# Optimization experiments

Hardware: AMD Instinct MI355X
Metric: run time of the kernel (lower is better)

The kernel has to match this reference:

```python
import jax, jax.numpy as jnp
import numpy as np

HIDDEN = 800
BETA = 0.95
SLOPE = 25.0

@jax.custom_vjp
def surrogate_spike(mem, thr):
    # hard threshold forward, sigmoid-derivative surrogate backward
    return (mem > thr).astype(mem.dtype)

def _spk_fwd(mem, thr):
    return surrogate_spike(mem, thr), (mem, thr)

def _spk_bwd(res, g):
    mem, thr = res
    s = jax.nn.sigmoid(SLOPE * (mem - thr))
    return (g * SLOPE * s * (1.0 - s), jnp.zeros_like(thr))

surrogate_spike.defvjp(_spk_fwd, _spk_bwd)


def setup_inputs() -> dict:
    key = jax.random.key(0)
    ks = jax.random.split(key, 6)
    T, B = 50, 512
    x = jax.random.normal(ks[0], (T, B, 784), dtype=jnp.float32)
    # Kaiming-ish init scaled by 1/sqrt(fan_in)
    W1 = jax.random.normal(ks[1], (HIDDEN, 784), dtype=jnp.float32) / np.sqrt(784.0)
    W2 = jax.random.normal(ks[2], (HIDDEN, HIDDEN), dtype=jnp.float32) / np.sqrt(float(HIDDEN))
    W3 = jax.random.normal(ks[3], (10, HIDDEN), dtype=jnp.float32) / np.sqrt(float(HIDDEN))
    b1 = jnp.zeros((HIDDEN,), jnp.float32)
    b2 = jnp.zeros((HIDDEN,), jnp.float32)
    b3 = jnp.zeros((10,), jnp.float32)
    budget1 = jax.random.uniform(ks[4], (HIDDEN,), dtype=jnp.float32)
    budget2 = jax.random.uniform(ks[5], (HIDDEN,), dtype=jnp.float32)
    return {"x": x, "W1": W1, "b1": b1, "W2": W2, "b2": b2,
            "W3": W3, "b3": b3, "budget1": budget1, "budget2": budget2}


def reference(x, W1, b1, W2, b2, W3, b3, budget1, budget2):
    # thresholds: 1 / clamp(budget / max_budget, 0.01, 1.0); max_budget = 1.0 here
    thr1 = 1.0 / jnp.clip(budget1, 0.01, 1.0)
    thr2 = 1.0 / jnp.clip(budget2, 0.01, 1.0)
    thr3 = jnp.asarray(1.0, x.dtype)
    B = x.shape[1]

    def step(carry, xt):
        m1, m2, m3 = carry
        m1 = BETA * m1 + xt @ W1.T + b1            # [B, HIDDEN]
        s1 = surrogate_spike(m1, thr1)
        m1 = m1 * (1.0 - s1)                        # multiplicative reset
        m2 = BETA * m2 + s1 @ W2.T + b2
        s2 = surrogate_spike(m2, thr2)
        m2 = m2 * (1.0 - s2)
        m3 = BETA * m3 + s2 @ W3.T + b3            # [B, 10]
        s3 = surrogate_spike(m3, thr3)
        m3 = m3 * (1.0 - s3)
        return (m1, m2, m3), (s1, s2, s3)

    init = (jnp.zeros((B, HIDDEN), x.dtype),
            jnp.zeros((B, HIDDEN), x.dtype),
            jnp.zeros((B, 10), x.dtype))
    _, (s1r, s2r, s3r) = jax.lax.scan(step, init, x)
    return (s3r.sum(0), s1r, s2r, s3r)
```

## Files before the change

### kernel.cpp

```cpp
#include <hip/hip_runtime.h>

#define BATCH   512
#define TSTEPS  50
#define NIN     784
#define NHID    800
#define NOUT    10
#define KC      384

#define BM 128
#define BN 64
#define BK 8

__global__ __launch_bounds__(256, 4)
void gemm_nt_f32(const float* __restrict__ A, const float* __restrict__ B,
                 float* __restrict__ C, int M, int N, int K)
{
    __shared__ float As[BK][BM + 4];
    __shared__ float Bs[BK][BN + 4];

    const int tid = threadIdx.x;
    const int tx = tid & 15;
    const int ty = tid >> 4;
    const int m0 = blockIdx.x * BM;
    const int n0 = blockIdx.y * BN;

    const int arow = tid >> 1;
    const int akq  = (tid & 1) * 4;
    const int brow = tid >> 2;
    const int bkq  = (tid & 3) * 2;

    const float* Aptr = A + (size_t)(m0 + arow) * K + akq;
    const float* Bptr = B + (size_t)(n0 + brow) * K + bkq;
    const bool bval = (n0 + brow) < N;

    float part[8][4];
    float acc[8][4];
    #pragma unroll
    for (int i = 0; i < 8; ++i)
        #pragma unroll
        for (int j = 0; j < 4; ++j) part[i][j] = 0.0f;

    float4 av = *(const float4*)(Aptr);
    float2 bv = bval ? *(const float2*)(Bptr) : make_float2(0.f, 0.f);

    for (int k0 = 0; k0 < K; k0 += BK) {
        __syncthreads();
        As[akq+0][arow] = av.x; As[akq+1][arow] = av.y;
        As[akq+2][arow] = av.z; As[akq+3][arow] = av.w;
        Bs[bkq+0][brow] = bv.x; Bs[bkq+1][brow] = bv.y;
        __syncthreads();

        if (k0 + BK < K) {
            av = *(const float4*)(Aptr + k0 + BK);
            bv = bval ? *(const float2*)(Bptr + k0 + BK) : make_float2(0.f, 0.f);
        }

        if (k0 == 384 || k0 == 768) {
            #pragma unroll
            for (int i = 0; i < 8; ++i)
                #pragma unroll
                for (int j = 0; j < 4; ++j) {
                    acc[i][j] = (k0 == 384) ? part[i][j]
                                            : __fadd_rn(acc[i][j], part[i][j]);
                    part[i][j] = 0.0f;
                }
        }

        #pragma unroll
        for (int kk = 0; kk < BK; ++kk) {
            float a[8], b[4];
            *(float4*)&a[0] = *(const float4*)&As[kk][8*ty];
            *(float4*)&a[4] = *(const float4*)&As[kk][8*ty + 4];
            *(float4*)&b[0] = *(const float4*)&Bs[kk][4*tx];
            #pragma unroll
            for (int i = 0; i < 8; ++i)
                #pragma unroll
                for (int j = 0; j < 4; ++j)
                    part[i][j] = __fmaf_rn(a[i], b[j], part[i][j]);
        }
    }

    #pragma unroll
    for (int i = 0; i < 8; ++i)
        #pragma unroll
        for (int j = 0; j < 4; ++j)
            acc[i][j] = (K <= KC) ? part[i][j] : __fadd_rn(acc[i][j], part[i][j]);

    const int cb = n0 + 4*tx;
    #pragma unroll
    for (int i = 0; i < 8; ++i) {
        const int m = m0 + 8*ty + i;
        float* crow = C + (size_t)m * N + cb;
        if (cb + 3 < N) {
            *(float4*)crow = make_float4(acc[i][0], acc[i][1], acc[i][2], acc[i][3]);
        } else {
            #pragma unroll
            for (int j = 0; j < 4; ++j)
                if (cb + j < N) crow[j] = acc[i][j];
        }
    }
}

__global__ __launch_bounds__(256)
void transpose800(const float* __restrict__ W2, float* __restrict__ W2T)
{
    __shared__ float t[32][33];
    const int tx  = threadIdx.x & 31;
    const int ty8 = threadIdx.x >> 5;
    const int bx = blockIdx.x * 32, by = blockIdx.y * 32;

    #pragma unroll
    for (int r = 0; r < 4; ++r) {
        int a = ty8 + r * 8;
        t[a][tx] = W2[(size_t)(by + a) * 800 + bx + tx];
    }
    __syncthreads();
    #pragma unroll
    for (int r = 0; r < 4; ++r) {
        int a = ty8 + r * 8;
        W2T[(size_t)(bx + a) * 800 + by + tx] = t[tx][a];
    }
}

__global__ __launch_bounds__(256)
void lif_scan_hid(const float* __restrict__ Z,
                  const float* __restrict__ bias,
                  const float* __restrict__ budget,
                  float* __restrict__ mcarry,
                  float* __restrict__ Sout,
                  unsigned long long* __restrict__ bm,
                  int CT, int t0)
{
    const int b = blockIdx.x;
    const int tid = threadIdx.x;
    const int lane = tid & 63;
    const int wave = tid >> 6;

    float m[4], thr[4], bj[4];
    bool val[4];
    #pragma unroll
    for (int c = 0; c < 4; ++c) {
        const int j = c * 256 + tid;
        val[c] = (j < NHID);
        const int jj = val[c] ? j : 0;
        float bu = budget[jj];
        bu = fminf(fmaxf(bu, 0.01f), 1.0f);
        thr[c] = __fdiv_rn(1.0f, bu);
        bj[c]  = bias[jj];
        m[c]   = mcarry[b * NHID + jj];
    }

    for (int ct = 0; ct < CT; ++ct) {
        const size_t zbase = (size_t)ct * (BATCH * NHID) + (size_t)b * NHID;
        const size_t sbase = (size_t)(t0 + ct) * (BATCH * NHID) + (size_t)b * NHID;
        #pragma unroll
        for (int c = 0; c < 4; ++c) {
            const int j = c * 256 + tid;
            bool sp = false;
            if (val[c]) {
                float z = Z[zbase + j];
                float mm = __fadd_rn(__fadd_rn(__fmul_rn(0.95f, m[c]), z), bj[c]);
                sp = (mm > thr[c]);
                m[c] = sp ? 0.0f : mm;
                Sout[sbase + j] = sp ? 1.0f : 0.0f;
            }
            unsigned long long bits = __ballot(sp);
            if (bm && lane == 0) {
                const int W = c * 4 + wave;
                if (W < 13)
                    bm[((size_t)ct * BATCH + b) * 13 + W] = bits;
            }
        }
    }
    #pragma unroll
    for (int c = 0; c < 4; ++c)
        if (val[c]) mcarry[b * NHID + c * 256 + tid] = m[c];
}

__global__ __launch_bounds__(256)
void spmm_spikes(const unsigned long long* __restrict__ bm,
                 const float* __restrict__ W2T,
                 float* __restrict__ Z,
                 int rows)
{
    __shared__ unsigned long long wbuf[13];
    __shared__ unsigned short list[NHID];
    __shared__ int offs[14];

    const int tid = threadIdx.x;
    const int lane = tid & 63;
    const int wave = tid >> 6;
    const int row = blockIdx.x;

    if (tid < 13) wbuf[tid] = bm[(size_t)row * 13 + tid];
    __syncthreads();
    if (tid == 0) {
        int o = 0;
        for (int w = 0; w < 13; ++w) { offs[w] = o; o += __popcll(wbuf[w]); }
        offs[13] = o;
    }
    __syncthreads();
    for (int W = wave; W < 13; W += 4) {
        const unsigned long long bits = wbuf[W];
        const int pre = __popcll(bits & ((1ull << lane) - 1ull));
        if ((bits >> lane) & 1ull)
            list[offs[W] + pre] = (unsigned short)(W * 64 + lane);
    }
    __syncthreads();
    const int nnz = offs[13];

    if (tid < 200) {
        const int n = 4 * tid;
        float p0 = 0.f, p1 = 0.f, p2 = 0.f, p3 = 0.f;
        float a0 = 0.f, a1 = 0.f, a2 = 0.f, a3 = 0.f;
        int p = 0, nextb = KC;
        for (int i = 0; i < nnz; ++i) {
            const int k = list[i];
            while (k >= nextb) {
                if (p == 0) { a0 = p0; a1 = p1; a2 = p2; a3 = p3; }
                else {
                    a0 = __fadd_rn(a0, p0); a1 = __fadd_rn(a1, p1);
                    a2 = __fadd_rn(a2, p2); a3 = __fadd_rn(a3, p3);
                }
                p0 = p1 = p2 = p3 = 0.f; ++p;
                nextb = (nextb == KC) ? 2 * KC : 100000;
            }
            const float4 w = *(const float4*)(W2T + (size_t)k * NHID + n);
            p0 = __fadd_rn(p0, w.x); p1 = __fadd_rn(p1, w.y);
            p2 = __fadd_rn(p2, w.z); p3 = __fadd_rn(p3, w.w);
        }
        while (p < 3) {
            if (p == 0) { a0 = p0; a1 = p1; a2 = p2; a3 = p3; }
            else {
                a0 = __fadd_rn(a0, p0); a1 = __fadd_rn(a1, p1);
                a2 = __fadd_rn(a2, p2); a3 = __fadd_rn(a3, p3);
            }
            p0 = p1 = p2 = p3 = 0.f; ++p;
        }
        *(float4*)(Z + (size_t)row * NHID + n) = make_float4(a0, a1, a2, a3);
    }
}

__global__ __launch_bounds__(256)
void gemm3_f32(const float* __restrict__ S2, const float* __restrict__ W3,
               float* __restrict__ Z3, int rows)
{
    int gid = blockIdx.x * 256 + threadIdx.x;
    if (gid >= rows * NOUT) return;
    const int m = gid / NOUT;
    const int n = gid % NOUT;
    const float* a = S2 + (size_t)m * NHID;
    const float* w = W3 + (size_t)n * NHID;

    float acc = 0.0f;
    for (int p0 = 0; p0 < NHID; p0 += KC) {
        const int pend = (p0 + KC < NHID) ? (p0 + KC) : NHID;
        float part = 0.0f;
        for (int k = p0; k < pend; ++k)
            part = __fmaf_rn(a[k], w[k], part);
        acc = (p0 == 0) ? part : __fadd_rn(acc, part);
    }
    Z3[gid] = acc;
}

__global__ __launch_bounds__(256)
void lif_scan_small(const float* __restrict__ Z, const float* __restrict__ bias,
                    float* __restrict__ mcarry, float* __restrict__ Sout,
                    int CT, int t0)
{
    const int idx = blockIdx.x * blockDim.x + threadIdx.x;
    const int total = BATCH * NOUT;
    if (idx >= total) return;
    const int j = idx % NOUT;
    const float thr = 1.0f;
    const float bj = bias[j];

    float m = mcarry[idx];
    for (int ct = 0; ct < CT; ++ct) {
        float z = Z[(size_t)ct * total + idx];
        m = __fadd_rn(__fadd_rn(__fmul_rn(0.95f, m), z), bj);
        float s;
        if (m > thr) { s = 1.0f; m = 0.0f; }
        else         { s = 0.0f; }
        Sout[(size_t)(t0 + ct) * total + idx] = s;
    }
    mcarry[idx] = m;
}

__global__ __launch_bounds__(256)
void sum_t(const float* __restrict__ S3, float* __restrict__ out0)
{
    const int idx = blockIdx.x * blockDim.x + threadIdx.x;
    if (idx >= BATCH * NOUT) return;
    float s = 0.0f;
    for (int t = 0; t < TSTEPS; ++t)
        s += S3[(size_t)t * BATCH * NOUT + idx];
    out0[idx] = s;
}

extern "C" void kernel_launch(void* const* d_in, const int* in_sizes, int n_in,
                              void* d_out, int out_size, void* d_ws, size_t ws_size,
                              hipStream_t stream)
{
    const float* x       = (const float*)d_in[0];
    const float* W1      = (const float*)d_in[1];
    const float* b1      = (const float*)d_in[2];
    const float* W2      = (const float*)d_in[3];
    const float* b2      = (const float*)d_in[4];
    const float* W3      = (const float*)d_in[5];
    const float* b3      = (const float*)d_in[6];
    const float* budget1 = (const float*)d_in[7];
    const float* budget2 = (const float*)d_in[8];

    float* out  = (float*)d_out;
    float* out0 = out;
    float* out1 = out0 + BATCH * NOUT;
    float* out2 = out1 + (size_t)TSTEPS * BATCH * NHID;
    float* out3 = out2 + (size_t)TSTEPS * BATCH * NHID;

    const size_t nBH = (size_t)BATCH * NHID;
    const size_t nBO = (size_t)BATCH * NOUT;
    float* m1c = (float*)d_ws;
    float* m2c = m1c + nBH;
    float* m3c = m2c + nBH;
    float* w2t = m3c + nBO;
    unsigned long long* bmask = (unsigned long long*)(w2t + (size_t)NHID * NHID);
    float* Z = (float*)(bmask + (size_t)TSTEPS * BATCH * 13);

    const size_t fixedF = 2 * nBH + nBO + (size_t)NHID * NHID
                        + (size_t)TSTEPS * BATCH * 13 * 2;
    size_t availF = (ws_size / 4 > fixedF) ? (ws_size / 4 - fixedF) : 0;
    const size_t perT = (size_t)BATCH * (NHID + NOUT);
    int CT = (int)(availF / perT);
    if (CT > TSTEPS) CT = TSTEPS;
    if (CT < 1) CT = 1;

    hipMemsetAsync(d_ws, 0, (2 * nBH + nBO) * sizeof(float), stream);

    {
        dim3 tg(25, 25);
        transpose800<<<tg, 256, 0, stream>>>(W2, w2t);
    }

    for (int t0 = 0; t0 < TSTEPS; t0 += CT) {
        int ct = TSTEPS - t0 < CT ? TSTEPS - t0 : CT;
        int Mrows = ct * BATCH;
        float* Z3 = Z + (size_t)ct * BATCH * NHID;

        {
            dim3 grid(Mrows / BM, (NHID + BN - 1) / BN);
            gemm_nt_f32<<<grid, 256, 0, stream>>>(
                x + (size_t)t0 * BATCH * NIN, W1, Z, Mrows, NHID, NIN);
        }
        lif_scan_hid<<<BATCH, 256, 0, stream>>>(
            Z, b1, budget1, m1c, out1, bmask, ct, t0);

        spmm_spikes<<<Mrows, 256, 0, stream>>>(bmask, w2t, Z, Mrows);
        lif_scan_hid<<<BATCH, 256, 0, stream>>>(
            Z, b2, budget2, m2c, out2, nullptr, ct, t0);

        gemm3_f32<<<(Mrows * NOUT + 255) / 256, 256, 0, stream>>>(
            out2 + (size_t)t0 * BATCH * NHID, W3, Z3, Mrows);
        lif_scan_small<<<(BATCH * NOUT + 255) / 256, 256, 0, stream>>>(
            Z3, b3, m3c, out3, ct, t0);
    }

    sum_t<<<(BATCH * NOUT + 255) / 256, 256, 0, stream>>>(out3, out0);
}
```

Before: 858.2 us.

## Split layer-1 GEMM into K-panel launches with larger tiles, sum panels in scan

Replaces the 128x64 FP32 GEMM, which kept its K-chunked partial sums in registers, with three separate launches over K ranges [0,384), [384,768) and [768,784). Each launch uses a 128x128 tile with an 8x8 per-thread micro-tile and writes its own partial buffer with nontemporal stores. The LIF scan kernel now reads the three partials and adds them, which keeps the same chunked summation order. This aims for more arithmetic per shared-memory load and drops the register cost of the extra accumulator. In exchange it triples Z traffic and workspace per timestep, so fewer timesteps fit in one chunk, and the last panel launch does very little work. Separately, gemm3 now uses vectorized float4 loads, and nontemporal hints are added to the scan's loads and stores.

Result: slower. 1.007 ms (+17.3%).

```diff
diff --git a/kernel.cpp b/kernel.cpp
--- a/kernel.cpp
+++ b/kernel.cpp
@@ -7,96 +7,79 @@
 #define NOUT    10
 #define KC      384
 
-#define BM 128
-#define BN 64
-#define BK 8
-
-__global__ __launch_bounds__(256, 4)
-void gemm_nt_f32(const float* __restrict__ A, const float* __restrict__ B,
-                 float* __restrict__ C, int M, int N, int K)
-{
-    __shared__ float As[BK][BM + 4];
-    __shared__ float Bs[BK][BN + 4];
+typedef float v4f __attribute__((ext_vector_type(4)));
+
+__global__ __launch_bounds__(256)
+void gemm_panel_f32(const float* __restrict__ A, const float* __restrict__ B,
+                    float* __restrict__ Cp, int M, int N, int K,
+                    int ks, int ke)
+{
+    __shared__ float As[8][132];
+    __shared__ float Bs[8][188];
 
     const int tid = threadIdx.x;
     const int tx = tid & 15;
     const int ty = tid >> 4;
-    const int m0 = blockIdx.x * BM;
-    const int n0 = blockIdx.y * BN;
-
-    const int arow = tid >> 1;
-    const int akq  = (tid & 1) * 4;
-    const int brow = tid >> 2;
-    const int bkq  = (tid & 3) * 2;
-
-    const float* Aptr = A + (size_t)(m0 + arow) * K + akq;
-    const float* Bptr = B + (size_t)(n0 + brow) * K + bkq;
-    const bool bval = (n0 + brow) < N;
-
-    float part[8][4];
-    float acc[8][4];
+    const int m0 = blockIdx.x * 128;
+    const int n0 = blockIdx.y * 128;
+
+    const int srow = tid >> 1;
+    const int skq  = (tid & 1) * 4;
+    const int bphys = 12 * (srow >> 3) + (srow & 7);
+
+    const float* Aptr = A + (size_t)(m0 + srow) * K + skq;
+    const float* Bptr = B + (size_t)(n0 + srow) * K + skq;
+    const bool bval = (n0 + srow) < N;
+
+    float part[8][8];
     #pragma unroll
     for (int i = 0; i < 8; ++i)
         #pragma unroll
-        for (int j = 0; j < 4; ++j) part[i][j] = 0.0f;
-
-    float4 av = *(const float4*)(Aptr);
-    float2 bv = bval ? *(const float2*)(Bptr) : make_float2(0.f, 0.f);
-
-    for (int k0 = 0; k0 < K; k0 += BK) {
+        for (int j = 0; j < 8; ++j) part[i][j] = 0.0f;
+
+    float4 av = *(const float4*)(Aptr + ks);
+    float4 bv = bval ? *(const float4*)(Bptr + ks) : make_float4(0.f,0.f,0.f,0.f);
+
+    for (int k0 = ks; k0 < ke; k0 += 8) {
         __syncthreads();
-        As[akq+0][arow] = av.x; As[akq+1][arow] = av.y;
-        As[akq+2][arow] = av.z; As[akq+3][arow] = av.w;
-        Bs[bkq+0][brow] = bv.x; Bs[bkq+1][brow] = bv.y;
+        As[skq+0][srow] = av.x; As[skq+1][srow] = av.y;
+        As[skq+2][srow] = av.z; As[skq+3][srow] = av.w;
+        Bs[skq+0][bphys] = bv.x; Bs[skq+1][bphys] = bv.y;
+        Bs[skq+2][bphys] = bv.z; Bs[skq+3][bphys] = bv.w;
         __syncthreads();
 
-        if (k0 + BK < K) {
-            av = *(const float4*)(Aptr + k0 + BK);
-            bv = bval ? *(const float2*)(Bptr + k0 + BK) : make_float2(0.f, 0.f);
-        }
-
-        if (k0 == 384 || k0 == 768) {
+        if (k0 + 8 < ke) {
+            av = *(const float4*)(Aptr + k0 + 8);
+            bv = bval ? *(const float4*)(Bptr + k0 + 8)
+                      : make_float4(0.f,0.f,0.f,0.f);
+        }
+
+        #pragma unroll
+        for (int kk = 0; kk < 8; ++kk) {
+            float a[8], b[8];
+            *(float4*)&a[0] = *(const float4*)&As[kk][8*ty];
+            *(float4*)&a[4] = *(const float4*)&As[kk][8*ty + 4];
+            *(float4*)&b[0] = *(const float4*)&Bs[kk][12*tx];
+            *(float4*)&b[4] = *(const float4*)&Bs[kk][12*tx + 4];
             #pragma unroll
             for (int i = 0; i < 8; ++i)
                 #pragma unroll
-                for (int j = 0; j < 4; ++j) {
-                    acc[i][j] = (k0 == 384) ? part[i][j]
-                                            : __fadd_rn(acc[i][j], part[i][j]);
-                    part[i][j] = 0.0f;
-                }
-        }
-
-        #pragma unroll
-        for (int kk = 0; kk < BK; ++kk) {
-            float a[8], b[4];
-            *(float4*)&a[0] = *(const float4*)&As[kk][8*ty];
-            *(float4*)&a[4] = *(const float4*)&As[kk][8*ty + 4];
-            *(float4*)&b[0] = *(const float4*)&Bs[kk][4*tx];
-            #pragma unroll
-            for (int i = 0; i < 8; ++i)
-                #pragma unroll
-                for (int j = 0; j < 4; ++j)
+                for (int j = 0; j < 8; ++j)
                     part[i][j] = __fmaf_rn(a[i], b[j], part[i][j]);
         }
     }
 
-    #pragma unroll
-    for (int i = 0; i < 8; ++i)
-        #pragma unroll
-        for (int j = 0; j < 4; ++j)
-            acc[i][j] = (K <= KC) ? part[i][j] : __fadd_rn(acc[i][j], part[i][j]);
-
-    const int cb = n0 + 4*tx;
+    const int cb = n0 + 8 * tx;
     #pragma unroll
     for (int i = 0; i < 8; ++i) {
-        const int m = m0 + 8*ty + i;
-        float* crow = C + (size_t)m * N + cb;
-        if (cb + 3 < N) {
-            *(float4*)crow = make_float4(acc[i][0], acc[i][1], acc[i][2], acc[i][3]);
-        } else {
-            #pragma unroll
-            for (int j = 0; j < 4; ++j)
-                if (cb + j < N) crow[j] = acc[i][j];
+        float* crow = Cp + (size_t)(m0 + 8*ty + i) * N + cb;
+        if (cb + 4 <= N) {
+            v4f o = { part[i][0], part[i][1], part[i][2], part[i][3] };
+            __builtin_nontemporal_store(o, (v4f*)crow);
+        }
+        if (cb + 8 <= N) {
+            v4f o = { part[i][4], part[i][5], part[i][6], part[i][7] };
+            __builtin_nontemporal_store(o, (v4f*)(crow + 4));
         }
     }
 }
@@ -123,7 +106,10 @@
 }
 
 __global__ __launch_bounds__(256)
-void lif_scan_hid(const float* __restrict__ Z,
+void lif_scan_hid(const float* __restrict__ Z0,
+                  const float* __restrict__ Z1,
+                  const float* __restrict__ Z2,
+                  int np,
                   const float* __restrict__ bias,
                   const float* __restrict__ budget,
                   float* __restrict__ mcarry,
@@ -158,11 +144,15 @@
             const int j = c * 256 + tid;
             bool sp = false;
             if (val[c]) {
-                float z = Z[zbase + j];
+                float z = __builtin_nontemporal_load(Z0 + zbase + j);
+                if (np >= 2)
+                    z = __fadd_rn(z, __builtin_nontemporal_load(Z1 + zbase + j));
+                if (np >= 3)
+                    z = __fadd_rn(z, __builtin_nontemporal_load(Z2 + zbase + j));
                 float mm = __fadd_rn(__fadd_rn(__fmul_rn(0.95f, m[c]), z), bj[c]);
                 sp = (mm > thr[c]);
                 m[c] = sp ? 0.0f : mm;
-                Sout[sbase + j] = sp ? 1.0f : 0.0f;
+                __builtin_nontemporal_store(sp ? 1.0f : 0.0f, Sout + sbase + j);
             }
             unsigned long long bits = __ballot(sp);
             if (bm && lane == 0) {
@@ -248,18 +238,25 @@
     int gid = blockIdx.x * 256 + threadIdx.x;
     if (gid >= rows * NOUT) return;
     const int m = gid / NOUT;
-    const int n = gid % NOUT;
+    const int nn = gid % NOUT;
     const float* a = S2 + (size_t)m * NHID;
-    const float* w = W3 + (size_t)n * NHID;
-
-    float acc = 0.0f;
-    for (int p0 = 0; p0 < NHID; p0 += KC) {
-        const int pend = (p0 + KC < NHID) ? (p0 + KC) : NHID;
-        float part = 0.0f;
-        for (int k = p0; k < pend; ++k)
-            part = __fmaf_rn(a[k], w[k], part);
-        acc = (p0 == 0) ? part : __fadd_rn(acc, part);
-    }
+    const float* wr = W3 + (size_t)nn * NHID;
+
+    float part = 0.0f, acc = 0.0f;
+    int p = 0;
+    for (int i = 0; i < NHID / 4; ++i) {
+        if (i == 96 || i == 192) {
+            acc = (p == 0) ? part : __fadd_rn(acc, part);
+            part = 0.0f; ++p;
+        }
+        const v4f a4 = __builtin_nontemporal_load((const v4f*)(a + 4 * i));
+        const float4 w4 = *(const float4*)(wr + 4 * i);
+        part = __fmaf_rn(a4.x, w4.x, part);
+        part = __fmaf_rn(a4.y, w4.y, part);
+        part = __fmaf_rn(a4.z, w4.z, part);
+        part = __fmaf_rn(a4.w, w4.w, part);
+    }
+    acc = (p == 0) ? part : __fadd_rn(acc, part);
     Z3[gid] = acc;
 }
 
@@ -330,7 +327,7 @@
     const size_t fixedF = 2 * nBH + nBO + (size_t)NHID * NHID
                         + (size_t)TSTEPS * BATCH * 13 * 2;
     size_t availF = (ws_size / 4 > fixedF) ? (ws_size / 4 - fixedF) : 0;
-    const size_t perT = (size_t)BATCH * (NHID + NOUT);
+    const size_t perT = (size_t)BATCH * (3 * NHID + NOUT);
     int CT = (int)(availF / perT);
     if (CT > TSTEPS) CT = TSTEPS;
     if (CT < 1) CT = 1;
@@ -345,19 +342,25 @@
     for (int t0 = 0; t0 < TSTEPS; t0 += CT) {
         int ct = TSTEPS - t0 < CT ? TSTEPS - t0 : CT;
         int Mrows = ct * BATCH;
-        float* Z3 = Z + (size_t)ct * BATCH * NHID;
+        const size_t pstride = (size_t)ct * BATCH * NHID;
+        float* Zp0 = Z;
+        float* Zp1 = Z + pstride;
+        float* Zp2 = Z + 2 * pstride;
+        float* Z3  = Z + 3 * pstride;
 
         {
-            dim3 grid(Mrows / BM, (NHID + BN - 1) / BN);
-            gemm_nt_f32<<<grid, 256, 0, stream>>>(
-                x + (size_t)t0 * BATCH * NIN, W1, Z, Mrows, NHID, NIN);
+            dim3 grid(Mrows / 128, (NHID + 127) / 128);
+            const float* xc = x + (size_t)t0 * BATCH * NIN;
+            gemm_panel_f32<<<grid, 256, 0, stream>>>(xc, W1, Zp0, Mrows, NHID, NIN, 0,   384);
+            gemm_panel_f32<<<grid, 256, 0, stream>>>(xc, W1, Zp1, Mrows, NHID, NIN, 384, 768);
+            gemm_panel_f32<<<grid, 256, 0, stream>>>(xc, W1, Zp2, Mrows, NHID, NIN, 768, 784);
         }
         lif_scan_hid<<<BATCH, 256, 0, stream>>>(
-            Z, b1, budget1, m1c, out1, bmask, ct, t0);
-
-        spmm_spikes<<<Mrows, 256, 0, stream>>>(bmask, w2t, Z, Mrows);
+            Zp0, Zp1, Zp2, 3, b1, budget1, m1c, out1, bmask, ct, t0);
+
+        spmm_spikes<<<Mrows, 256, 0, stream>>>(bmask, w2t, Zp0, Mrows);
         lif_scan_hid<<<BATCH, 256, 0, stream>>>(
-            Z, b2, budget2, m2c, out2, nullptr, ct, t0);
+            Zp0, nullptr, nullptr, 1, b2, budget2, m2c, out2, nullptr, ct, t0);
 
         gemm3_f32<<<(Mrows * NOUT + 255) / 256, 256, 0, stream>>>(
             out2 + (size_t)t0 * BATCH * NHID, W3, Z3, Mrows);
```
